# Kernel optimization log

Hardware: AMD Instinct MI355X
Metric: run time of the kernel (lower is better)

Reference implementation:

```python
import jax, jax.numpy as jnp
import numpy as np

N, C, HD = 8192, 1024, 128

def setup_inputs() -> dict:
    key = jax.random.key(0)
    ks = jax.random.split(key, 9)
    def xavier(k, fan_in, fan_out):
        lim = float(np.sqrt(6.0 / (fan_in + fan_out)))
        return jax.random.uniform(k, (fan_out, fan_in), jnp.float32, -lim, lim)
    return {
        "x": jax.random.normal(ks[0], (N, C), jnp.float32),
        "Wq": xavier(ks[1], C, HD), "bq": jnp.zeros((HD,), jnp.float32),
        "Wk": xavier(ks[2], C, HD), "bk": jnp.zeros((HD,), jnp.float32),
        "Wv": xavier(ks[3], C, C),  "bv": jnp.zeros((C,), jnp.float32),
        "Wo": xavier(ks[4], C, C),  "bo": jnp.zeros((C,), jnp.float32),
    }

def reference(x, Wq, bq, Wk, bk, Wv, bv, Wo, bo):
    scale = HD ** -0.5
    q = x @ Wq.T + bq          # (N, HD)
    k = x @ Wk.T + bk          # (N, HD)
    v = x @ Wv.T + bv          # (N, C)
    scores = (q @ k.T) * scale # (N, N)
    attn = jax.nn.softmax(scores, axis=-1)
    out = attn @ v             # (N, C)
    return out @ Wo.T + bo
```

## Files before the change

kernel.cpp:

```cpp
#include <hip/hip_runtime.h>

#define NTOK 8192
#define CDIM 1024
#define HDIM 128

typedef __attribute__((ext_vector_type(8))) short short8;
typedef __attribute__((ext_vector_type(4))) float floatx4;
typedef __attribute__((ext_vector_type(16))) float floatx16;

__device__ inline unsigned short f2bf(float f) {
    union { float f; unsigned u; } v; v.f = f;
    unsigned r = v.u + 0x7fffu + ((v.u >> 16) & 1u);
    return (unsigned short)(r >> 16);
}
__device__ inline float bf2f(short s) {
    union { unsigned u; float f; } v;
    v.u = ((unsigned)(unsigned short)s) << 16;
    return v.f;
}
__device__ inline void async16(const unsigned short* g, short* l) {
    __builtin_amdgcn_global_load_lds(
        (const __attribute__((address_space(1))) unsigned*)g,
        (__attribute__((address_space(3))) unsigned*)l, 16, 0, 0);
}

__global__ void cast_f32_bf16(const float* __restrict__ in,
                              unsigned short* __restrict__ out, int n4) {
    int i = blockIdx.x * blockDim.x + threadIdx.x;
    if (i < n4) {
        float4 v = ((const float4*)in)[i];
        ushort4 o;
        o.x = f2bf(v.x); o.y = f2bf(v.y); o.z = f2bf(v.z); o.w = f2bf(v.w);
        ((ushort4*)out)[i] = o;
    }
}

__global__ __launch_bounds__(256) void gemm_qk(
    const unsigned short* __restrict__ A,
    const unsigned short* __restrict__ Wq, const float* __restrict__ bq,
    const unsigned short* __restrict__ Wk, const float* __restrict__ bk,
    unsigned short* __restrict__ qout, unsigned short* __restrict__ kout, int K)
{
    __shared__ short As[4][64][8];
    __shared__ short Ws[4][64][8];
    const int tid = threadIdx.x;
    const int wave = tid >> 6, lane = tid & 63;
    const int lr = lane & 15, lc = lane >> 4;
    const int m0 = blockIdx.x * 64;
    const int isK = blockIdx.y >> 1;
    const int n0 = (blockIdx.y & 1) * 64;
    const unsigned short* W = isK ? Wk : Wq;
    const float* bias = isK ? bk : bq;

    floatx4 acc[4] = {};
    const int srow = tid >> 2, sch = tid & 3;
    const unsigned short* Ag = A + (long)(m0 + srow) * K + sch * 8;
    const unsigned short* Wg = W + (long)(n0 + srow) * K + sch * 8;

    for (int k0 = 0; k0 < K; k0 += 32) {
        *(short8*)&As[sch][srow][0] = *(const short8*)(Ag + k0);
        *(short8*)&Ws[sch][srow][0] = *(const short8*)(Wg + k0);
        __syncthreads();
        short8 a = *(short8*)&As[lc][wave * 16 + lr][0];
#pragma unroll
        for (int s = 0; s < 4; s++) {
            short8 b = *(short8*)&Ws[lc][s * 16 + lr][0];
            acc[s] = __builtin_amdgcn_mfma_f32_16x16x32_bf16(a, b, acc[s], 0, 0, 0);
        }
        __syncthreads();
    }

#pragma unroll
    for (int s = 0; s < 4; s++) {
        int h = n0 + s * 16 + lr;
        float bv = bias[h];
        int tok0 = m0 + wave * 16 + lc * 4;
#pragma unroll
        for (int r = 0; r < 4; r++) {
            int tok = tok0 + r;
            if (isK)
                kout[(tok >> 5) * 4096 + (h >> 3) * 256 + (tok & 31) * 8 + (h & 7)] =
                    f2bf(acc[s][r] + bv);
            else
                qout[(long)tok * HDIM + h] = f2bf(acc[s][r] + bv);
        }
    }
}

template<int MODE>
__global__ __launch_bounds__(256) void gemm128_nt(
    const unsigned short* __restrict__ A, const unsigned short* __restrict__ W,
    const float* __restrict__ bias, void* __restrict__ out, int M, int N, int K)
{
    __shared__ short As[128][4][8];
    __shared__ short Ws[128][4][8];
    const int tid = threadIdx.x, wave = tid >> 6, lane = tid & 63;
    const int lr = lane & 15, lc = lane >> 4;
    const int wm = (wave >> 1) * 64, wn = (wave & 1) * 64;
    const int m0 = blockIdx.x * 128, n0 = blockIdx.y * 128;

    floatx4 acc[4][4] = {};

    const int srow = lane >> 2, sch = lane & 3;
    const unsigned short* Ag0 = A + (long)(m0 + wave * 32 + srow) * K + sch * 8;
    const unsigned short* Ag1 = Ag0 + (long)16 * K;
    const unsigned short* Wg0 = W + (long)(n0 + wave * 32 + srow) * K + sch * 8;
    const unsigned short* Wg1 = Wg0 + (long)16 * K;
    short* lA0 = &As[wave * 32][0][0];
    short* lA1 = &As[wave * 32 + 16][0][0];
    short* lW0 = &Ws[wave * 32][0][0];
    short* lW1 = &Ws[wave * 32 + 16][0][0];

    for (int k0 = 0; k0 < K; k0 += 32) {
        async16(Ag0 + k0, lA0);
        async16(Ag1 + k0, lA1);
        async16(Wg0 + k0, lW0);
        async16(Wg1 + k0, lW1);
        __syncthreads();
        short8 af[4], bfg[4];
#pragma unroll
        for (int i = 0; i < 4; i++) af[i]  = *(short8*)&As[wm + i * 16 + lr][lc][0];
#pragma unroll
        for (int j = 0; j < 4; j++) bfg[j] = *(short8*)&Ws[wn + j * 16 + lr][lc][0];
#pragma unroll
        for (int i = 0; i < 4; i++)
#pragma unroll
            for (int j = 0; j < 4; j++)
                acc[i][j] = __builtin_amdgcn_mfma_f32_16x16x32_bf16(af[i], bfg[j], acc[i][j], 0, 0, 0);
        __syncthreads();
    }

#pragma unroll
    for (int i = 0; i < 4; i++) {
        int t0 = m0 + wm + i * 16 + lc * 4;
#pragma unroll
        for (int j = 0; j < 4; j++) {
            int c = n0 + wn + j * 16 + lr;
            float bv = bias[c];
            if (MODE == 0) {
                float* o = (float*)out;
#pragma unroll
                for (int r = 0; r < 4; r++) o[(long)(t0 + r) * N + c] = acc[i][j][r] + bv;
            } else {
                unsigned short* o = (unsigned short*)out;
                ushort4 pk;
                pk.x = f2bf(acc[i][j][0] + bv); pk.y = f2bf(acc[i][j][1] + bv);
                pk.z = f2bf(acc[i][j][2] + bv); pk.w = f2bf(acc[i][j][3] + bv);
                long off = (long)(c >> 8) * 2097152 + (t0 >> 5) * 8192 +
                           ((t0 & 31) >> 3) * 2048 + (c & 255) * 8 + (t0 & 7);
                *(ushort4*)&o[off] = pk;
            }
        }
    }
}

__global__ __launch_bounds__(512, 2) void attn_pv(
    const unsigned short* __restrict__ qb, const unsigned short* __restrict__ ksw,
    const unsigned short* __restrict__ vsw,
    unsigned short* __restrict__ Oa, unsigned short* __restrict__ Ob,
    float* __restrict__ la, float* __restrict__ lb)
{
    __shared__ short Ks[3][8192];
    __shared__ short Vs[3][16384];

    const int tid = threadIdx.x, wave = tid >> 6, lane = tid & 63;
    const int l31 = lane & 31, h = lane >> 5;
    const int m0 = blockIdx.x * 256, cblk = blockIdx.y;
    const int mw = m0 + wave * 32;
    const int nt0 = blockIdx.z * 128;
    unsigned short* Op = blockIdx.z ? Ob : Oa;
    float* ls = blockIdx.z ? lb : la;
    const float cexp = (float)(0.08838834764831845 * 1.4426950408889634);

    short8 qf[8];
#pragma unroll
    for (int kk = 0; kk < 8; kk++)
        qf[kk] = *(const short8*)&qb[(mw + l31) * HDIM + kk * 16 + h * 8];

    floatx16 acc[8] = {};
    float ls0 = 0.f, ls1 = 0.f, ls2 = 0.f, ls3 = 0.f;

    const unsigned short* kg0 = ksw + (wave * 2 + 0) * 512 + lane * 8;
    const unsigned short* kg1 = ksw + (wave * 2 + 1) * 512 + lane * 8;
    const unsigned short* vgb = vsw + (long)cblk * 2097152 + lane * 8;
    const unsigned short* vg0 = vgb + (wave * 4 + 0) * 512;
    const unsigned short* vg1 = vgb + (wave * 4 + 1) * 512;
    const unsigned short* vg2 = vgb + (wave * 4 + 2) * 512;
    const unsigned short* vg3 = vgb + (wave * 4 + 3) * 512;

    short* kr = &Ks[0][0];
    short* kw = &Ks[1][0];
    short* k2 = &Ks[2][0];
    short* vr = &Vs[0][0];
    short* vw = &Vs[1][0];
    short* v2 = &Vs[2][0];

#define STAGE(P, KD, VD)                                                \
    {                                                                   \
        long ok_ = (long)(nt0 + 2 * (P)) * 4096;                        \
        long ov_ = (long)(nt0 + 2 * (P)) * 8192;                        \
        async16(kg0 + ok_, (KD) + (wave * 2 + 0) * 512);                \
        async16(kg1 + ok_, (KD) + (wave * 2 + 1) * 512);                \
        async16(vg0 + ov_, (VD) + (wave * 4 + 0) * 512);                \
        async16(vg1 + ov_, (VD) + (wave * 4 + 1) * 512);                \
        async16(vg2 + ov_, (VD) + (wave * 4 + 2) * 512);                \
        async16(vg3 + ov_, (VD) + (wave * 4 + 3) * 512);                \
    }

    STAGE(0, kr, vr);

    for (int p = 0; p < 64; ++p) {
        if (p + 1 < 64) STAGE(p + 1, kw, vw);
        __builtin_amdgcn_sched_barrier(0);
        if (p == 63) asm volatile("s_waitcnt vmcnt(0)" ::: "memory");
        else         asm volatile("s_waitcnt vmcnt(6)" ::: "memory");
        __builtin_amdgcn_sched_barrier(0);
        __builtin_amdgcn_s_barrier();
        __builtin_amdgcn_sched_barrier(0);

#pragma unroll
        for (int t = 0; t < 2; t++) {
            short* kb = kr + t * 4096;
            short* vb = vr + t * 8192;

            floatx16 st = {};
            __builtin_amdgcn_s_setprio(1);
#pragma unroll
            for (int kk = 0; kk < 8; kk++) {
                short8 kf = *(short8*)(kb + (kk * 2 + h) * 256 + l31 * 8);
                st = __builtin_amdgcn_mfma_f32_32x32x16_bf16(kf, qf[kk], st, 0, 0, 0);
            }
            __builtin_amdgcn_s_setprio(0);

            unsigned pk0, pk1, pk2, pk3, pk4, pk5, pk6, pk7;
            {
                float p0, p1;
#define PK(I, DST, LS) \
                p0 = __builtin_amdgcn_exp2f(st[2 * I] * cexp); \
                p1 = __builtin_amdgcn_exp2f(st[2 * I + 1] * cexp); \
                LS += p0 + p1; \
                asm("v_cvt_pk_bf16_f32 %0, %1, %2" : "=v"(DST) : "v"(p0), "v"(p1));
                PK(0, pk0, ls0) PK(1, pk1, ls1) PK(2, pk2, ls2) PK(3, pk3, ls3)
                PK(4, pk4, ls0) PK(5, pk5, ls1) PK(6, pk6, ls2) PK(7, pk7, ls3)
#undef PK
            }
            asm("v_permlane32_swap_b32 %0, %1" : "+v"(pk0), "+v"(pk2));
            asm("v_permlane32_swap_b32 %0, %1" : "+v"(pk1), "+v"(pk3));
            asm("v_permlane32_swap_b32 %0, %1" : "+v"(pk4), "+v"(pk6));
            asm("v_permlane32_swap_b32 %0, %1" : "+v"(pk5), "+v"(pk7));
            union { unsigned u[4]; short8 s; } up0, up1;
            up0.u[0] = pk0; up0.u[1] = pk1; up0.u[2] = pk2; up0.u[3] = pk3;
            up1.u[0] = pk4; up1.u[1] = pk5; up1.u[2] = pk6; up1.u[3] = pk7;
            const short8 pa0 = up0.s, pa1 = up1.s;

            __builtin_amdgcn_s_setprio(1);
#pragma unroll
            for (int ct = 0; ct < 8; ct++) {
                short8 bv0 = *(short8*)(vb + h * 2048 + (ct * 32 + l31) * 8);
                short8 bv1 = *(short8*)(vb + (2 + h) * 2048 + (ct * 32 + l31) * 8);
                acc[ct] = __builtin_amdgcn_mfma_f32_32x32x16_bf16(pa0, bv0, acc[ct], 0, 0, 0);
                acc[ct] = __builtin_amdgcn_mfma_f32_32x32x16_bf16(pa1, bv1, acc[ct], 0, 0, 0);
            }
            __builtin_amdgcn_s_setprio(0);
        }

        short* t0 = kr; kr = kw; kw = k2; k2 = t0;
        short* t1 = vr; vr = vw; vw = v2; v2 = t1;
    }
#undef STAGE

#pragma unroll
    for (int ct = 0; ct < 8; ct++) {
        int c = cblk * 256 + ct * 32 + l31;
#pragma unroll
        for (int r = 0; r < 16; r++) {
            int q = (r & 3) + 8 * (r >> 2) + 4 * h;
            Op[(long)(mw + q) * CDIM + c] = f2bf(acc[ct][r]);
        }
    }
    if (blockIdx.y == 0) {
        float lsum = (ls0 + ls1) + (ls2 + ls3);
        lsum += __shfl_xor(lsum, 32);
        if (lane < 32) ls[mw + lane] = lsum;
    }
}

__global__ __launch_bounds__(256) void combine_attn(
    const unsigned short* __restrict__ Oa, unsigned short* __restrict__ Ob,
    const float* __restrict__ la, const float* __restrict__ lb)
{
    int i = blockIdx.x * blockDim.x + threadIdx.x;
    int row = i >> 7;
    float inv = 1.0f / (la[row] + lb[row]);
    short8 a = ((const short8*)Oa)[i];
    short8 b = ((const short8*)Ob)[i];
    short8 o;
#pragma unroll
    for (int e = 0; e < 8; e++) o[e] = (short)f2bf((bf2f(a[e]) + bf2f(b[e])) * inv);
    ((short8*)Ob)[i] = o;
}

extern "C" void kernel_launch(void* const* d_in, const int* in_sizes, int n_in,
                              void* d_out, int out_size, void* d_ws, size_t ws_size,
                              hipStream_t stream) {
    const float* x  = (const float*)d_in[0];
    const float* Wq = (const float*)d_in[1];
    const float* bq = (const float*)d_in[2];
    const float* Wk = (const float*)d_in[3];
    const float* bk = (const float*)d_in[4];
    const float* Wv = (const float*)d_in[5];
    const float* bv = (const float*)d_in[6];
    const float* Wo = (const float*)d_in[7];
    const float* bo = (const float*)d_in[8];

    char* ws = (char*)d_ws;
    unsigned short* x_bf   = (unsigned short*)(ws + 0);
    unsigned short* wq_bf  = (unsigned short*)(ws + 16777216);
    unsigned short* wk_bf  = (unsigned short*)(ws + 17039360);
    unsigned short* wv_bf  = (unsigned short*)(ws + 17301504);
    unsigned short* wo_bf  = (unsigned short*)(ws + 19398656);
    unsigned short* q_bf   = (unsigned short*)(ws + 21495808);
    unsigned short* k_swz  = (unsigned short*)(ws + 23592960);
    unsigned short* v_swz  = (unsigned short*)(ws + 25690112);
    unsigned short* attn_bf= (unsigned short*)(ws + 42467328);
    float* lsum_a          = (float*)(ws + 59244544);
    float* lsum_b          = (float*)(ws + 59277312);

    cast_f32_bf16<<<8192, 256, 0, stream>>>(x,  x_bf,  2097152);
    cast_f32_bf16<<<128,  256, 0, stream>>>(Wq, wq_bf, 32768);
    cast_f32_bf16<<<128,  256, 0, stream>>>(Wk, wk_bf, 32768);
    cast_f32_bf16<<<1024, 256, 0, stream>>>(Wv, wv_bf, 262144);
    cast_f32_bf16<<<1024, 256, 0, stream>>>(Wo, wo_bf, 262144);

    gemm_qk<<<dim3(128, 4), 256, 0, stream>>>(x_bf, wq_bf, bq, wk_bf, bk,
                                              q_bf, k_swz, CDIM);
    gemm128_nt<2><<<dim3(64, 8), 256, 0, stream>>>(x_bf, wv_bf, bv, v_swz, NTOK, CDIM, CDIM);

    attn_pv<<<dim3(32, 4, 2), 512, 0, stream>>>(q_bf, k_swz, v_swz,
                                                x_bf, attn_bf, lsum_a, lsum_b);
    combine_attn<<<4096, 256, 0, stream>>>(x_bf, attn_bf, lsum_a, lsum_b);

    gemm128_nt<0><<<dim3(64, 8), 256, 0, stream>>>(attn_bf, wo_bf, bo, d_out, NTOK, CDIM, CDIM);
}
```

Before: 373.3 us.

## Fuse casts, double-buffer 128-tile GEMM, interleave two QK tiles in attention

Merges the five f32-to-bf16 cast launches into one kernel that picks its source by block range, removing launch overhead. The 128x128 GEMM now double-buffers its LDS tiles and issues the next tile's async loads right after the barrier, overlapping loads with MFMA and dropping one barrier per k-step. The attention inner loop computes both QK score tiles together, then both exp/pack steps, then both PV steps, giving the scheduler more independent MFMA work at the cost of extra registers.

New measurement: 358.8 us. 3.9% less time.

```diff
diff --git a/kernel.cpp b/kernel.cpp
--- a/kernel.cpp
+++ b/kernel.cpp
@@ -24,15 +24,26 @@
         (__attribute__((address_space(3))) unsigned*)l, 16, 0, 0);
 }
 
-__global__ void cast_f32_bf16(const float* __restrict__ in,
-                              unsigned short* __restrict__ out, int n4) {
-    int i = blockIdx.x * blockDim.x + threadIdx.x;
-    if (i < n4) {
-        float4 v = ((const float4*)in)[i];
-        ushort4 o;
-        o.x = f2bf(v.x); o.y = f2bf(v.y); o.z = f2bf(v.z); o.w = f2bf(v.w);
-        ((ushort4*)out)[i] = o;
-    }
+__global__ __launch_bounds__(256) void cast_all(
+    const float* __restrict__ x,  const float* __restrict__ Wv,
+    const float* __restrict__ Wo, const float* __restrict__ Wq,
+    const float* __restrict__ Wk,
+    unsigned short* __restrict__ xo, unsigned short* __restrict__ wvo,
+    unsigned short* __restrict__ woo, unsigned short* __restrict__ wqo,
+    unsigned short* __restrict__ wko)
+{
+    int b = blockIdx.x;
+    const float* in; unsigned short* out; int base;
+    if (b < 8192)       { in = x;  out = xo;  base = b; }
+    else if (b < 9216)  { in = Wv; out = wvo; base = b - 8192; }
+    else if (b < 10240) { in = Wo; out = woo; base = b - 9216; }
+    else if (b < 10368) { in = Wq; out = wqo; base = b - 10240; }
+    else                { in = Wk; out = wko; base = b - 10368; }
+    int i = base * 256 + threadIdx.x;
+    float4 v = ((const float4*)in)[i];
+    ushort4 o;
+    o.x = f2bf(v.x); o.y = f2bf(v.y); o.z = f2bf(v.z); o.w = f2bf(v.w);
+    ((ushort4*)out)[i] = o;
 }
 
 __global__ __launch_bounds__(256) void gemm_qk(
@@ -92,8 +103,8 @@
     const unsigned short* __restrict__ A, const unsigned short* __restrict__ W,
     const float* __restrict__ bias, void* __restrict__ out, int M, int N, int K)
 {
-    __shared__ short As[128][4][8];
-    __shared__ short Ws[128][4][8];
+    __shared__ short As[2][128][4][8];
+    __shared__ short Ws[2][128][4][8];
     const int tid = threadIdx.x, wave = tid >> 6, lane = tid & 63;
     const int lr = lane & 15, lc = lane >> 4;
     const int wm = (wave >> 1) * 64, wn = (wave & 1) * 64;
@@ -106,29 +117,32 @@
     const unsigned short* Ag1 = Ag0 + (long)16 * K;
     const unsigned short* Wg0 = W + (long)(n0 + wave * 32 + srow) * K + sch * 8;
     const unsigned short* Wg1 = Wg0 + (long)16 * K;
-    short* lA0 = &As[wave * 32][0][0];
-    short* lA1 = &As[wave * 32 + 16][0][0];
-    short* lW0 = &Ws[wave * 32][0][0];
-    short* lW1 = &Ws[wave * 32 + 16][0][0];
-
-    for (int k0 = 0; k0 < K; k0 += 32) {
-        async16(Ag0 + k0, lA0);
-        async16(Ag1 + k0, lA1);
-        async16(Wg0 + k0, lW0);
-        async16(Wg1 + k0, lW1);
+
+#define GSTAGE(K0, S)                                        \
+    {                                                        \
+        async16(Ag0 + (K0), &As[S][wave * 32][0][0]);        \
+        async16(Ag1 + (K0), &As[S][wave * 32 + 16][0][0]);   \
+        async16(Wg0 + (K0), &Ws[S][wave * 32][0][0]);        \
+        async16(Wg1 + (K0), &Ws[S][wave * 32 + 16][0][0]);   \
+    }
+
+    GSTAGE(0, 0);
+    int s = 0;
+    for (int k0 = 0; k0 < K; k0 += 32, s ^= 1) {
         __syncthreads();
+        if (k0 + 32 < K) GSTAGE(k0 + 32, s ^ 1);
         short8 af[4], bfg[4];
 #pragma unroll
-        for (int i = 0; i < 4; i++) af[i]  = *(short8*)&As[wm + i * 16 + lr][lc][0];
-#pragma unroll
-        for (int j = 0; j < 4; j++) bfg[j] = *(short8*)&Ws[wn + j * 16 + lr][lc][0];
+        for (int i = 0; i < 4; i++) af[i]  = *(short8*)&As[s][wm + i * 16 + lr][lc][0];
+#pragma unroll
+        for (int j = 0; j < 4; j++) bfg[j] = *(short8*)&Ws[s][wn + j * 16 + lr][lc][0];
 #pragma unroll
         for (int i = 0; i < 4; i++)
 #pragma unroll
             for (int j = 0; j < 4; j++)
                 acc[i][j] = __builtin_amdgcn_mfma_f32_16x16x32_bf16(af[i], bfg[j], acc[i][j], 0, 0, 0);
-        __syncthreads();
-    }
+    }
+#undef GSTAGE
 
 #pragma unroll
     for (int i = 0; i < 4; i++) {
@@ -209,63 +223,99 @@
 
     STAGE(0, kr, vr);
 
-    for (int p = 0; p < 64; ++p) {
-        if (p + 1 < 64) STAGE(p + 1, kw, vw);
+    for (int ph = 0; ph < 64; ++ph) {
+        if (ph + 1 < 64) STAGE(ph + 1, kw, vw);
         __builtin_amdgcn_sched_barrier(0);
-        if (p == 63) asm volatile("s_waitcnt vmcnt(0)" ::: "memory");
-        else         asm volatile("s_waitcnt vmcnt(6)" ::: "memory");
+        if (ph == 63) asm volatile("s_waitcnt vmcnt(0)" ::: "memory");
+        else          asm volatile("s_waitcnt vmcnt(6)" ::: "memory");
         __builtin_amdgcn_sched_barrier(0);
         __builtin_amdgcn_s_barrier();
         __builtin_amdgcn_sched_barrier(0);
 
-#pragma unroll
-        for (int t = 0; t < 2; t++) {
-            short* kb = kr + t * 4096;
-            short* vb = vr + t * 8192;
-
-            floatx16 st = {};
-            __builtin_amdgcn_s_setprio(1);
-#pragma unroll
-            for (int kk = 0; kk < 8; kk++) {
-                short8 kf = *(short8*)(kb + (kk * 2 + h) * 256 + l31 * 8);
-                st = __builtin_amdgcn_mfma_f32_32x32x16_bf16(kf, qf[kk], st, 0, 0, 0);
-            }
-            __builtin_amdgcn_s_setprio(0);
-
-            unsigned pk0, pk1, pk2, pk3, pk4, pk5, pk6, pk7;
-            {
-                float p0, p1;
-#define PK(I, DST, LS) \
-                p0 = __builtin_amdgcn_exp2f(st[2 * I] * cexp); \
-                p1 = __builtin_amdgcn_exp2f(st[2 * I + 1] * cexp); \
-                LS += p0 + p1; \
-                asm("v_cvt_pk_bf16_f32 %0, %1, %2" : "=v"(DST) : "v"(p0), "v"(p1));
-                PK(0, pk0, ls0) PK(1, pk1, ls1) PK(2, pk2, ls2) PK(3, pk3, ls3)
-                PK(4, pk4, ls0) PK(5, pk5, ls1) PK(6, pk6, ls2) PK(7, pk7, ls3)
-#undef PK
-            }
-            asm("v_permlane32_swap_b32 %0, %1" : "+v"(pk0), "+v"(pk2));
-            asm("v_permlane32_swap_b32 %0, %1" : "+v"(pk1), "+v"(pk3));
-            asm("v_permlane32_swap_b32 %0, %1" : "+v"(pk4), "+v"(pk6));
-            asm("v_permlane32_swap_b32 %0, %1" : "+v"(pk5), "+v"(pk7));
-            union { unsigned u[4]; short8 s; } up0, up1;
-            up0.u[0] = pk0; up0.u[1] = pk1; up0.u[2] = pk2; up0.u[3] = pk3;
-            up1.u[0] = pk4; up1.u[1] = pk5; up1.u[2] = pk6; up1.u[3] = pk7;
-            const short8 pa0 = up0.s, pa1 = up1.s;
-
-            __builtin_amdgcn_s_setprio(1);
-#pragma unroll
-            for (int ct = 0; ct < 8; ct++) {
-                short8 bv0 = *(short8*)(vb + h * 2048 + (ct * 32 + l31) * 8);
-                short8 bv1 = *(short8*)(vb + (2 + h) * 2048 + (ct * 32 + l31) * 8);
-                acc[ct] = __builtin_amdgcn_mfma_f32_32x32x16_bf16(pa0, bv0, acc[ct], 0, 0, 0);
-                acc[ct] = __builtin_amdgcn_mfma_f32_32x32x16_bf16(pa1, bv1, acc[ct], 0, 0, 0);
-            }
-            __builtin_amdgcn_s_setprio(0);
-        }
-
-        short* t0 = kr; kr = kw; kw = k2; k2 = t0;
-        short* t1 = vr; vr = vw; vw = v2; v2 = t1;
+        short* kb0 = kr;        short* vb0 = vr;
+        short* kb1 = kr + 4096; short* vb1 = vr + 8192;
+
+        floatx16 st0 = {}, st1 = {};
+        __builtin_amdgcn_s_setprio(1);
+#pragma unroll
+        for (int kk = 0; kk < 8; kk++) {
+            short8 kf0 = *(short8*)(kb0 + (kk * 2 + h) * 256 + l31 * 8);
+            short8 kf1 = *(short8*)(kb1 + (kk * 2 + h) * 256 + l31 * 8);
+            st0 = __builtin_amdgcn_mfma_f32_32x32x16_bf16(kf0, qf[kk], st0, 0, 0, 0);
+            st1 = __builtin_amdgcn_mfma_f32_32x32x16_bf16(kf1, qf[kk], st1, 0, 0, 0);
+        }
+        __builtin_amdgcn_s_setprio(0);
+
+#define EXP_PACK(ST, PA0, PA1)                                                      \
+        short8 PA0, PA1;                                                            \
+        {                                                                           \
+            unsigned pk0, pk1, pk2, pk3, pk4, pk5, pk6, pk7;                        \
+            float p0, p1;                                                           \
+            _Pragma("clang diagnostic push")                                        \
+            p0 = __builtin_amdgcn_exp2f(ST[0] * cexp);                              \
+            p1 = __builtin_amdgcn_exp2f(ST[1] * cexp);                              \
+            ls0 += p0 + p1;                                                         \
+            asm("v_cvt_pk_bf16_f32 %0, %1, %2" : "=v"(pk0) : "v"(p0), "v"(p1));     \
+            p0 = __builtin_amdgcn_exp2f(ST[2] * cexp);                              \
+            p1 = __builtin_amdgcn_exp2f(ST[3] * cexp);                              \
+            ls1 += p0 + p1;                                                         \
+            asm("v_cvt_pk_bf16_f32 %0, %1, %2" : "=v"(pk1) : "v"(p0), "v"(p1));     \
+            p0 = __builtin_amdgcn_exp2f(ST[4] * cexp);                              \
+            p1 = __builtin_amdgcn_exp2f(ST[5] * cexp);                              \
+            ls2 += p0 + p1;                                                         \
+            asm("v_cvt_pk_bf16_f32 %0, %1, %2" : "=v"(pk2) : "v"(p0), "v"(p1));     \
+            p0 = __builtin_amdgcn_exp2f(ST[6] * cexp);                              \
+            p1 = __builtin_amdgcn_exp2f(ST[7] * cexp);                              \
+            ls3 += p0 + p1;                                                         \
+            asm("v_cvt_pk_bf16_f32 %0, %1, %2" : "=v"(pk3) : "v"(p0), "v"(p1));     \
+            p0 = __builtin_amdgcn_exp2f(ST[8] * cexp);                              \
+            p1 = __builtin_amdgcn_exp2f(ST[9] * cexp);                              \
+            ls0 += p0 + p1;                                                         \
+            asm("v_cvt_pk_bf16_f32 %0, %1, %2" : "=v"(pk4) : "v"(p0), "v"(p1));     \
+            p0 = __builtin_amdgcn_exp2f(ST[10] * cexp);                             \
+            p1 = __builtin_amdgcn_exp2f(ST[11] * cexp);                             \
+            ls1 += p0 + p1;                                                         \
+            asm("v_cvt_pk_bf16_f32 %0, %1, %2" : "=v"(pk5) : "v"(p0), "v"(p1));     \
+            p0 = __builtin_amdgcn_exp2f(ST[12] * cexp);                             \
+            p1 = __builtin_amdgcn_exp2f(ST[13] * cexp);                             \
+            ls2 += p0 + p1;                                                         \
+            asm("v_cvt_pk_bf16_f32 %0, %1, %2" : "=v"(pk6) : "v"(p0), "v"(p1));     \
+            p0 = __builtin_amdgcn_exp2f(ST[14] * cexp);                             \
+            p1 = __builtin_amdgcn_exp2f(ST[15] * cexp);                             \
+            ls3 += p0 + p1;                                                         \
+            asm("v_cvt_pk_bf16_f32 %0, %1, %2" : "=v"(pk7) : "v"(p0), "v"(p1));     \
+            _Pragma("clang diagnostic pop")                                         \
+            asm("v_permlane32_swap_b32 %0, %1" : "+v"(pk0), "+v"(pk2));             \
+            asm("v_permlane32_swap_b32 %0, %1" : "+v"(pk1), "+v"(pk3));             \
+            asm("v_permlane32_swap_b32 %0, %1" : "+v"(pk4), "+v"(pk6));             \
+            asm("v_permlane32_swap_b32 %0, %1" : "+v"(pk5), "+v"(pk7));             \
+            union { unsigned u[4]; short8 s; } up0_, up1_;                          \
+            up0_.u[0] = pk0; up0_.u[1] = pk1; up0_.u[2] = pk2; up0_.u[3] = pk3;     \
+            up1_.u[0] = pk4; up1_.u[1] = pk5; up1_.u[2] = pk6; up1_.u[3] = pk7;     \
+            PA0 = up0_.s; PA1 = up1_.s;                                             \
+        }
+
+#define PV(VB, PA0, PA1)                                                            \
+        __builtin_amdgcn_s_setprio(1);                                              \
+        _Pragma("unroll")                                                           \
+        for (int ct = 0; ct < 8; ct++) {                                            \
+            short8 bv0 = *(short8*)((VB) + h * 2048 + (ct * 32 + l31) * 8);         \
+            short8 bv1 = *(short8*)((VB) + (2 + h) * 2048 + (ct * 32 + l31) * 8);   \
+            acc[ct] = __builtin_amdgcn_mfma_f32_32x32x16_bf16(PA0, bv0, acc[ct], 0, 0, 0); \
+            acc[ct] = __builtin_amdgcn_mfma_f32_32x32x16_bf16(PA1, bv1, acc[ct], 0, 0, 0); \
+        }                                                                           \
+        __builtin_amdgcn_s_setprio(0);
+
+        EXP_PACK(st0, pa0_0, pa1_0)
+        EXP_PACK(st1, pa0_1, pa1_1)
+        PV(vb0, pa0_0, pa1_0)
+        PV(vb1, pa0_1, pa1_1)
+
+#undef EXP_PACK
+#undef PV
+
+        short* t0p = kr; kr = kw; kw = k2; k2 = t0p;
+        short* t1p = vr; vr = vw; vw = v2; v2 = t1p;
     }
 #undef STAGE
 
@@ -326,11 +376,8 @@
     float* lsum_a          = (float*)(ws + 59244544);
     float* lsum_b          = (float*)(ws + 59277312);
 
-    cast_f32_bf16<<<8192, 256, 0, stream>>>(x,  x_bf,  2097152);
-    cast_f32_bf16<<<128,  256, 0, stream>>>(Wq, wq_bf, 32768);
-    cast_f32_bf16<<<128,  256, 0, stream>>>(Wk, wk_bf, 32768);
-    cast_f32_bf16<<<1024, 256, 0, stream>>>(Wv, wv_bf, 262144);
-    cast_f32_bf16<<<1024, 256, 0, stream>>>(Wo, wo_bf, 262144);
+    cast_all<<<10496, 256, 0, stream>>>(x, Wv, Wo, Wq, Wk,
+                                        x_bf, wv_bf, wo_bf, wq_bf, wk_bf);
 
     gemm_qk<<<dim3(128, 4), 256, 0, stream>>>(x_bf, wq_bf, bq, wk_bf, bk,
                                               q_bf, k_swz, CDIM);
```
